# Optimization experiments

Measured on AMD Instinct MI355X. Metric: run time of the kernel, lower is better.

## Reference

```python
import jax, jax.numpy as jnp
import numpy as np

B, T = 32768, 32
OBJ_V, PRED_V = 179, 46
E_OBJ, E_PRED, H = 5, 5, 32
IN_DIM = E_OBJ + E_PRED + 2 + 4  # 16, matches LSTMCell input size


def setup_inputs() -> dict:
    key = jax.random.key(0)
    ks = jax.random.split(key, 12)
    s = 0.1
    return {
        "input_objects": jax.random.randint(ks[0], (B, T), 0, OBJ_V),
        "input_boxes": jax.random.uniform(ks[1], (B, T, 4), dtype=jnp.float32),
        "predicates": jax.random.randint(ks[2], (B, T), 0, PRED_V),
        "subject_indicators": jax.random.randint(ks[3], (B, T), 0, 2),
        "target_object": jax.random.randint(ks[4], (B,), 0, OBJ_V),
        "obj_emb": jax.random.normal(ks[5], (OBJ_V, E_OBJ), dtype=jnp.float32) * s,
        "pred_emb": jax.random.normal(ks[6], (PRED_V, E_PRED), dtype=jnp.float32) * s,
        "W_ih": jax.random.normal(ks[7], (4 * H, IN_DIM), dtype=jnp.float32) * s,
        "W_hh": jax.random.normal(ks[8], (4 * H, H), dtype=jnp.float32) * s,
        "b_ih": jnp.zeros((4 * H,), dtype=jnp.float32),
        "b_hh": jnp.zeros((4 * H,), dtype=jnp.float32),
        "fc2_W": jax.random.normal(ks[9], (4, H), dtype=jnp.float32) * s,
        "fc2_b": jnp.zeros((4,), dtype=jnp.float32),
    }


def _forward(input_objects, input_boxes, predicates, subject_indicators,
             obj_emb, pred_emb, W_ih, W_hh, b_ih, b_hh, fc2_W, fc2_b):
    # concatenate_features, vectorized over all timesteps at once: [B,T,16]
    feats = jnp.concatenate([
        obj_emb[input_objects],                                   # [B,T,5]
        pred_emb[predicates],                                     # [B,T,5]
        jax.nn.one_hot(subject_indicators, 2, dtype=jnp.float32), # [B,T,2]
        input_boxes,                                              # [B,T,4]
    ], axis=-1)
    xs = jnp.transpose(feats, (1, 0, 2))  # [T,B,16] for scan over time

    def step(carry, x):
        h, c = carry
        gates = x @ W_ih.T + b_ih + h @ W_hh.T + b_hh  # [B,4H]
        i, f, g, o = jnp.split(gates, 4, axis=-1)      # torch gate order i,f,g,o
        i = jax.nn.sigmoid(i)
        f = jax.nn.sigmoid(f)
        g = jnp.tanh(g)
        o = jax.nn.sigmoid(o)
        c = f * c + i * g
        h = o * jnp.tanh(c)
        return (h, c), None

    h0 = jnp.zeros((input_objects.shape[0], H), dtype=jnp.float32)
    (h, _), _ = jax.lax.scan(step, (h0, h0), xs)
    out = h @ fc2_W.T + fc2_b          # output_fc2 on last hidden state
    return jnp.clip(out, 0.0, 1.0)     # torch.clamp(min=0, max=1)


def reference(input_objects, input_boxes, predicates, subject_indicators, target_object,
              obj_emb, pred_emb, W_ih, W_hh, b_ih, b_hh, fc2_W, fc2_b):
    # target_object is accepted by the torch forward but unused in its body
    return _forward(input_objects, input_boxes, predicates, subject_indicators,
                    obj_emb, pred_emb, W_ih, W_hh, b_ih, b_hh, fc2_W, fc2_b)
```

## Files before the change

### kernel.cpp

```cpp
#include <hip/hip_runtime.h>

#define LDS_BYTES 38416

typedef _Float16 f16x8 __attribute__((ext_vector_type(8)));
typedef float    f32x4 __attribute__((ext_vector_type(4)));

__device__ __forceinline__ float fast_sigmoid(float x) {
    float e = __builtin_amdgcn_exp2f(x * -1.44269504088896f);
    return __builtin_amdgcn_rcpf(1.0f + e);
}
__device__ __forceinline__ float fast_tanh(float x) {
    float e = __builtin_amdgcn_exp2f(x * 2.88539008177793f);
    return 1.0f - 2.0f * __builtin_amdgcn_rcpf(1.0f + e);
}

__global__ __launch_bounds__(256, 4)
void lstm_fused(const int* __restrict__ objs,
                const float* __restrict__ boxes,
                const int* __restrict__ preds,
                const int* __restrict__ subj,
                const float* __restrict__ obj_emb,
                const float* __restrict__ pred_emb,
                const float* __restrict__ W_ih,
                const float* __restrict__ W_hh,
                const float* __restrict__ b_ih,
                const float* __restrict__ b_hh,
                const float* __restrict__ fc2_W,
                const float* __restrict__ fc2_b,
                float* __restrict__ out)
{
    extern __shared__ char smem[];
    const int tid   = threadIdx.x;
    const int lane  = tid & 63;
    const int wv    = tid >> 6;
    const int quad  = lane >> 4;
    const int cidx  = lane & 15;
    const int jhalf = wv & 1;
    const int Mt    = wv >> 1;

    const int XOFF = 0, HOFF = 33280, ZOFF = 38400;

    {
        int* z = (int*)(smem + HOFF);
        for (int i = tid; i < 1284; i += 256) z[i] = 0;
    }

    {
        int b  = tid >> 3;
        int t0 = (tid & 7) << 2;
        long gb = (long)blockIdx.x * 32 + b;
        int4 ov = *(const int4*)(objs  + gb * 32 + t0);
        int4 pv = *(const int4*)(preds + gb * 32 + t0);
        int4 sv = *(const int4*)(subj  + gb * 32 + t0);
        int oarr[4] = {ov.x, ov.y, ov.z, ov.w};
        int parr[4] = {pv.x, pv.y, pv.z, pv.w};
        int sarr[4] = {sv.x, sv.y, sv.z, sv.w};
        #pragma unroll
        for (int tt = 0; tt < 4; ++tt) {
            int t = t0 + tt;
            const float* eo = obj_emb  + oarr[tt] * 5;
            const float* ep = pred_emb + parr[tt] * 5;
            float4 bx = *(const float4*)(boxes + (gb * 32 + t) * 4);
            f16x8 lo, hi;
            lo[0]=(_Float16)eo[0]; lo[1]=(_Float16)eo[1]; lo[2]=(_Float16)eo[2];
            lo[3]=(_Float16)eo[3]; lo[4]=(_Float16)eo[4];
            lo[5]=(_Float16)ep[0]; lo[6]=(_Float16)ep[1]; lo[7]=(_Float16)ep[2];
            hi[0]=(_Float16)ep[3]; hi[1]=(_Float16)ep[4];
            hi[2]=(_Float16)(sarr[tt]==0 ? 1.0f : 0.0f);
            hi[3]=(_Float16)(sarr[tt]==1 ? 1.0f : 0.0f);
            hi[4]=(_Float16)bx.x; hi[5]=(_Float16)bx.y;
            hi[6]=(_Float16)bx.z; hi[7]=(_Float16)bx.w;
            char* dst = smem + XOFF + b * 1040 + t * 32;
            *(f16x8*)dst        = lo;
            *(f16x8*)(dst + 16) = hi;
        }
    }

    f16x8 Wf[4][2];
    float biasv[4];
    #pragma unroll
    for (int g = 0; g < 4; ++g) {
        int n = (jhalf + 2 * g) * 16 + cidx;
        biasv[g] = b_ih[n] + b_hh[n];
        #pragma unroll
        for (int ks = 0; ks < 2; ++ks) {
            f16x8 v;
            #pragma unroll
            for (int jj = 0; jj < 8; ++jj) {
                int k = ks * 32 + quad * 8 + jj;
                float val = (k < 16) ? W_ih[n * 16 + k]
                          : (k < 48) ? W_hh[n * 32 + (k - 16)]
                          : 0.0f;
                v[jj] = (_Float16)val;
            }
            Wf[g][ks] = v;
        }
    }

    const int  m_a  = Mt * 16 + cidx;
    const bool isx0 = (quad < 2);
    const int  a0x  = XOFF + m_a * 1040 + quad * 16;
    const int  a0h  = HOFF + m_a * 80 + (quad - 2) * 16;
    const int  a1h  = HOFF + m_a * 80 + 32 + quad * 16;
    const int  b_row0 = Mt * 16 + quad * 4;
    const int  kh     = jhalf * 16 + cidx;
    const int  wrb_base = HOFF + b_row0 * 80 + kh * 2;

    float cst[4] = {0.f, 0.f, 0.f, 0.f};
    float hl[4]  = {0.f, 0.f, 0.f, 0.f};

    __syncthreads();

    for (int t = 0; t < 32; ++t) {
        int sel  = (t & 1) * 2560;
        int off0 = isx0 ? (a0x + t * 32) : (a0h + sel);
        int off1 = isx0 ? (a1h + sel)    : ZOFF;
        f16x8 a0 = *(const f16x8*)(smem + off0);
        f16x8 a1 = *(const f16x8*)(smem + off1);

        f32x4 acc[4];
        #pragma unroll
        for (int g = 0; g < 4; ++g) {
            float bv = biasv[g];
            f32x4 a = {bv, bv, bv, bv};
            a = __builtin_amdgcn_mfma_f32_16x16x32_f16(a0, Wf[g][0], a, 0, 0, 0);
            a = __builtin_amdgcn_mfma_f32_16x16x32_f16(a1, Wf[g][1], a, 0, 0, 0);
            acc[g] = a;
        }

        int wrb = wrb_base + ((t + 1) & 1) * 2560;
        #pragma unroll
        for (int r = 0; r < 4; ++r) {
            float iv = acc[0][r], fv = acc[1][r], gv = acc[2][r], ovl = acc[3][r];
            float si = fast_sigmoid(iv);
            float sf = fast_sigmoid(fv);
            float tg = fast_tanh(gv);
            float so = fast_sigmoid(ovl);
            float cn = sf * cst[r] + si * tg;
            cst[r] = cn;
            float hv = so * fast_tanh(cn);
            hl[r] = hv;
            *(_Float16*)(smem + wrb + 80 * r) = (_Float16)hv;
        }
        __syncthreads();
    }

    #pragma unroll
    for (int r = 0; r < 4; ++r)
        *(float*)(smem + (b_row0 + r) * 132 + kh * 4) = hl[r];
    __syncthreads();

    if (tid < 128) {
        int b = tid >> 2, jj = tid & 3;
        const float* fw   = fc2_W + jj * 32;
        const float* hrow = (const float*)smem + b * 33;
        float s = fc2_b[jj];
        #pragma unroll
        for (int k = 0; k < 32; ++k) s += fw[k] * hrow[k];
        s = fminf(fmaxf(s, 0.0f), 1.0f);
        out[((long)blockIdx.x * 32 + b) * 4 + jj] = s;
    }
}

extern "C" void kernel_launch(void* const* d_in, const int* in_sizes, int n_in,
                              void* d_out, int out_size, void* d_ws, size_t ws_size,
                              hipStream_t stream)
{
    lstm_fused<<<1024, 256, LDS_BYTES, stream>>>(
        (const int*)d_in[0], (const float*)d_in[1], (const int*)d_in[2],
        (const int*)d_in[3],
        (const float*)d_in[5], (const float*)d_in[6],
        (const float*)d_in[7], (const float*)d_in[8],
        (const float*)d_in[9], (const float*)d_in[10],
        (const float*)d_in[11], (const float*)d_in[12],
        (float*)d_out);
}
```

Baseline: 155.6 us.

## Run each LSTM block as one wave to drop per-step barriers

Result: no change. 154.8 us (-0.5%).

```diff
diff --git a/kernel.cpp b/kernel.cpp
--- a/kernel.cpp
+++ b/kernel.cpp
@@ -1,20 +1,21 @@
 #include <hip/hip_runtime.h>
 
-#define LDS_BYTES 38416
+#define LDS_BYTES 17952
 
 typedef _Float16 f16x8 __attribute__((ext_vector_type(8)));
 typedef float    f32x4 __attribute__((ext_vector_type(4)));
 
-__device__ __forceinline__ float fast_sigmoid(float x) {
-    float e = __builtin_amdgcn_exp2f(x * -1.44269504088896f);
-    return __builtin_amdgcn_rcpf(1.0f + e);
+#define LOG2E     1.44269504088896f
+#define TWO_LOG2E 2.88539008177793f
+
+__device__ __forceinline__ float sig_pre(float a) {
+    return __builtin_amdgcn_rcpf(1.0f + __builtin_amdgcn_exp2f(a));
 }
-__device__ __forceinline__ float fast_tanh(float x) {
-    float e = __builtin_amdgcn_exp2f(x * 2.88539008177793f);
-    return 1.0f - 2.0f * __builtin_amdgcn_rcpf(1.0f + e);
+__device__ __forceinline__ float tanh_pre(float a) {
+    return 1.0f - 2.0f * __builtin_amdgcn_rcpf(1.0f + __builtin_amdgcn_exp2f(a));
 }
 
-__global__ __launch_bounds__(256, 4)
+__global__ __launch_bounds__(64, 2)
 void lstm_fused(const int* __restrict__ objs,
                 const float* __restrict__ boxes,
                 const int* __restrict__ preds,
@@ -30,58 +31,65 @@
                 float* __restrict__ out)
 {
     extern __shared__ char smem[];
-    const int tid   = threadIdx.x;
-    const int lane  = tid & 63;
-    const int wv    = tid >> 6;
-    const int quad  = lane >> 4;
-    const int cidx  = lane & 15;
-    const int jhalf = wv & 1;
-    const int Mt    = wv >> 1;
-
-    const int XOFF = 0, HOFF = 33280, ZOFF = 38400;
+    const int tid  = threadIdx.x;
+    const int quad = tid >> 4;
+    const int cidx = tid & 15;
+    const int XOFF = 0, HOFF = 16640, ZOFF = 17920;
 
     {
         int* z = (int*)(smem + HOFF);
-        for (int i = tid; i < 1284; i += 256) z[i] = 0;
+        #pragma unroll
+        for (int i = 0; i < 6; ++i) {
+            int idx = tid + i * 64;
+            if (idx < 328) z[idx] = 0;
+        }
     }
 
     {
-        int b  = tid >> 3;
-        int t0 = (tid & 7) << 2;
-        long gb = (long)blockIdx.x * 32 + b;
-        int4 ov = *(const int4*)(objs  + gb * 32 + t0);
-        int4 pv = *(const int4*)(preds + gb * 32 + t0);
-        int4 sv = *(const int4*)(subj  + gb * 32 + t0);
-        int oarr[4] = {ov.x, ov.y, ov.z, ov.w};
-        int parr[4] = {pv.x, pv.y, pv.z, pv.w};
-        int sarr[4] = {sv.x, sv.y, sv.z, sv.w};
+        int b  = tid >> 2;
+        int t0 = (tid & 3) << 3;
+        long gb = (long)blockIdx.x * 16 + b;
+        const int* op = objs  + gb * 32 + t0;
+        const int* pp = preds + gb * 32 + t0;
+        const int* sp = subj  + gb * 32 + t0;
         #pragma unroll
-        for (int tt = 0; tt < 4; ++tt) {
-            int t = t0 + tt;
-            const float* eo = obj_emb  + oarr[tt] * 5;
-            const float* ep = pred_emb + parr[tt] * 5;
-            float4 bx = *(const float4*)(boxes + (gb * 32 + t) * 4);
-            f16x8 lo, hi;
-            lo[0]=(_Float16)eo[0]; lo[1]=(_Float16)eo[1]; lo[2]=(_Float16)eo[2];
-            lo[3]=(_Float16)eo[3]; lo[4]=(_Float16)eo[4];
-            lo[5]=(_Float16)ep[0]; lo[6]=(_Float16)ep[1]; lo[7]=(_Float16)ep[2];
-            hi[0]=(_Float16)ep[3]; hi[1]=(_Float16)ep[4];
-            hi[2]=(_Float16)(sarr[tt]==0 ? 1.0f : 0.0f);
-            hi[3]=(_Float16)(sarr[tt]==1 ? 1.0f : 0.0f);
-            hi[4]=(_Float16)bx.x; hi[5]=(_Float16)bx.y;
-            hi[6]=(_Float16)bx.z; hi[7]=(_Float16)bx.w;
-            char* dst = smem + XOFF + b * 1040 + t * 32;
-            *(f16x8*)dst        = lo;
-            *(f16x8*)(dst + 16) = hi;
+        for (int c = 0; c < 8; c += 4) {
+            int4 ov = *(const int4*)(op + c);
+            int4 pv = *(const int4*)(pp + c);
+            int4 sv = *(const int4*)(sp + c);
+            int oarr[4] = {ov.x, ov.y, ov.z, ov.w};
+            int parr[4] = {pv.x, pv.y, pv.z, pv.w};
+            int sarr[4] = {sv.x, sv.y, sv.z, sv.w};
+            #pragma unroll
+            for (int tt = 0; tt < 4; ++tt) {
+                int t = t0 + c + tt;
+                const float* eo = obj_emb  + oarr[tt] * 5;
+                const float* ep = pred_emb + parr[tt] * 5;
+                float4 bx = *(const float4*)(boxes + (gb * 32 + t) * 4);
+                f16x8 lo, hi;
+                lo[0]=(_Float16)eo[0]; lo[1]=(_Float16)eo[1]; lo[2]=(_Float16)eo[2];
+                lo[3]=(_Float16)eo[3]; lo[4]=(_Float16)eo[4];
+                lo[5]=(_Float16)ep[0]; lo[6]=(_Float16)ep[1]; lo[7]=(_Float16)ep[2];
+                hi[0]=(_Float16)ep[3]; hi[1]=(_Float16)ep[4];
+                hi[2]=(_Float16)(sarr[tt]==0 ? 1.0f : 0.0f);
+                hi[3]=(_Float16)(sarr[tt]==1 ? 1.0f : 0.0f);
+                hi[4]=(_Float16)bx.x; hi[5]=(_Float16)bx.y;
+                hi[6]=(_Float16)bx.z; hi[7]=(_Float16)bx.w;
+                char* dst = smem + XOFF + b * 1040 + t * 32;
+                *(f16x8*)dst        = lo;
+                *(f16x8*)(dst + 16) = hi;
+            }
         }
     }
 
-    f16x8 Wf[4][2];
-    float biasv[4];
+    f16x8 Wf[8][2];
+    f32x4 bias4[8];
     #pragma unroll
-    for (int g = 0; g < 4; ++g) {
-        int n = (jhalf + 2 * g) * 16 + cidx;
-        biasv[g] = b_ih[n] + b_hh[n];
+    for (int j = 0; j < 8; ++j) {
+        int n = j * 16 + cidx;
+        float scale = (j >= 4 && j < 6) ? TWO_LOG2E : -LOG2E;
+        float bv = (b_ih[n] + b_hh[n]) * scale;
+        bias4[j] = (f32x4){bv, bv, bv, bv};
         #pragma unroll
         for (int ks = 0; ks < 2; ++ks) {
             f16x8 v;
@@ -91,74 +99,80 @@
                 float val = (k < 16) ? W_ih[n * 16 + k]
                           : (k < 48) ? W_hh[n * 32 + (k - 16)]
                           : 0.0f;
-                v[jj] = (_Float16)val;
+                v[jj] = (_Float16)(val * scale);
             }
-            Wf[g][ks] = v;
+            Wf[j][ks] = v;
         }
     }
 
-    const int  m_a  = Mt * 16 + cidx;
-    const bool isx0 = (quad < 2);
-    const int  a0x  = XOFF + m_a * 1040 + quad * 16;
-    const int  a0h  = HOFF + m_a * 80 + (quad - 2) * 16;
-    const int  a1h  = HOFF + m_a * 80 + 32 + quad * 16;
-    const int  b_row0 = Mt * 16 + quad * 4;
-    const int  kh     = jhalf * 16 + cidx;
-    const int  wrb_base = HOFF + b_row0 * 80 + kh * 2;
+    const bool isx  = (quad < 2);
+    int addr0 = isx ? (XOFF + cidx * 1040 + quad * 16)
+                    : (HOFF + cidx * 80 + (quad - 2) * 16);
+    const int inc0  = isx ? 32 : 0;
+    const int addr1 = isx ? (HOFF + cidx * 80 + 32 + quad * 16)
+                          : ZOFF;
+    const int wr_b  = quad * 4;
 
-    float cst[4] = {0.f, 0.f, 0.f, 0.f};
-    float hl[4]  = {0.f, 0.f, 0.f, 0.f};
+    float cst[8] = {0,0,0,0,0,0,0,0};
+    float hl[8];
 
     __syncthreads();
 
+    #pragma unroll 4
     for (int t = 0; t < 32; ++t) {
-        int sel  = (t & 1) * 2560;
-        int off0 = isx0 ? (a0x + t * 32) : (a0h + sel);
-        int off1 = isx0 ? (a1h + sel)    : ZOFF;
-        f16x8 a0 = *(const f16x8*)(smem + off0);
-        f16x8 a1 = *(const f16x8*)(smem + off1);
+        f16x8 a0 = *(const f16x8*)(smem + addr0);
+        f16x8 a1 = *(const f16x8*)(smem + addr1);
+        addr0 += inc0;
 
-        f32x4 acc[4];
+        f32x4 acc[8];
         #pragma unroll
-        for (int g = 0; g < 4; ++g) {
-            float bv = biasv[g];
-            f32x4 a = {bv, bv, bv, bv};
-            a = __builtin_amdgcn_mfma_f32_16x16x32_f16(a0, Wf[g][0], a, 0, 0, 0);
-            a = __builtin_amdgcn_mfma_f32_16x16x32_f16(a1, Wf[g][1], a, 0, 0, 0);
-            acc[g] = a;
+        for (int j = 0; j < 8; ++j) {
+            f32x4 a = __builtin_amdgcn_mfma_f32_16x16x32_f16(a0, Wf[j][0], bias4[j], 0, 0, 0);
+            acc[j]  = __builtin_amdgcn_mfma_f32_16x16x32_f16(a1, Wf[j][1], a, 0, 0, 0);
         }
 
-        int wrb = wrb_base + ((t + 1) & 1) * 2560;
         #pragma unroll
         for (int r = 0; r < 4; ++r) {
-            float iv = acc[0][r], fv = acc[1][r], gv = acc[2][r], ovl = acc[3][r];
-            float si = fast_sigmoid(iv);
-            float sf = fast_sigmoid(fv);
-            float tg = fast_tanh(gv);
-            float so = fast_sigmoid(ovl);
-            float cn = sf * cst[r] + si * tg;
-            cst[r] = cn;
-            float hv = so * fast_tanh(cn);
-            hl[r] = hv;
-            *(_Float16*)(smem + wrb + 80 * r) = (_Float16)hv;
+            float si0 = sig_pre(acc[0][r]);
+            float si1 = sig_pre(acc[1][r]);
+            float sf0 = sig_pre(acc[2][r]);
+            float sf1 = sig_pre(acc[3][r]);
+            float tg0 = tanh_pre(acc[4][r]);
+            float tg1 = tanh_pre(acc[5][r]);
+            float so0 = sig_pre(acc[6][r]);
+            float so1 = sig_pre(acc[7][r]);
+            float c0 = fmaf(sf0, cst[2*r],   si0 * tg0);
+            float c1 = fmaf(sf1, cst[2*r+1], si1 * tg1);
+            cst[2*r] = c0; cst[2*r+1] = c1;
+            float h0 = so0 * tanh_pre(c0 * TWO_LOG2E);
+            float h1 = so1 * tanh_pre(c1 * TWO_LOG2E);
+            hl[2*r] = h0; hl[2*r+1] = h1;
+            *(_Float16*)(smem + HOFF + (wr_b + r) * 80 + cidx * 2)      = (_Float16)h0;
+            *(_Float16*)(smem + HOFF + (wr_b + r) * 80 + 32 + cidx * 2) = (_Float16)h1;
         }
-        __syncthreads();
     }
 
+    __syncthreads();
     #pragma unroll
-    for (int r = 0; r < 4; ++r)
-        *(float*)(smem + (b_row0 + r) * 132 + kh * 4) = hl[r];
+    for (int r = 0; r < 4; ++r) {
+        *(float*)(smem + (wr_b + r) * 144 + cidx * 4)      = hl[2*r];
+        *(float*)(smem + (wr_b + r) * 144 + 64 + cidx * 4) = hl[2*r+1];
+    }
     __syncthreads();
 
-    if (tid < 128) {
+    {
         int b = tid >> 2, jj = tid & 3;
         const float* fw   = fc2_W + jj * 32;
-        const float* hrow = (const float*)smem + b * 33;
+        const float* hrow = (const float*)(smem + b * 144);
         float s = fc2_b[jj];
         #pragma unroll
-        for (int k = 0; k < 32; ++k) s += fw[k] * hrow[k];
+        for (int k = 0; k < 8; ++k) {
+            float4 hv = *(const float4*)(hrow + k * 4);
+            s += fw[k*4+0] * hv.x + fw[k*4+1] * hv.y
+               + fw[k*4+2] * hv.z + fw[k*4+3] * hv.w;
+        }
         s = fminf(fmaxf(s, 0.0f), 1.0f);
-        out[((long)blockIdx.x * 32 + b) * 4 + jj] = s;
+        out[(long)blockIdx.x * 64 + tid] = s;
     }
 }
 
@@ -166,7 +180,7 @@
                               void* d_out, int out_size, void* d_ws, size_t ws_size,
                               hipStream_t stream)
 {
-    lstm_fused<<<1024, 256, LDS_BYTES, stream>>>(
+    lstm_fused<<<2048, 64, LDS_BYTES, stream>>>(
         (const int*)d_in[0], (const float*)d_in[1], (const int*)d_in[2],
         (const int*)d_in[3],
         (const float*)d_in[5], (const float*)d_in[6],
```
